# Kernel tuning notes

Measured on AMD Instinct MI355X. Metric: run time of the kernel, lower is better.

Reference implementation:

```python
import jax, jax.numpy as jnp
import numpy as np

NUM_CLASSES = 81
THRESHOLD = 0.5
NEGPOS_RATIO = 3
VARIANCE = (0.1, 0.2)


def point_form(p):
    # center-size -> corner form
    return jnp.concatenate([p[:, :2] - p[:, 2:] / 2, p[:, :2] + p[:, 2:] / 2], axis=1)


def jaccard(box_a, box_b):
    # box_a: [O,4] corners, box_b: [P,4] corners -> IoU [O,P]
    lt = jnp.maximum(box_a[:, None, :2], box_b[None, :, :2])
    rb = jnp.minimum(box_a[:, None, 2:], box_b[None, :, 2:])
    wh = jnp.clip(rb - lt, 0.0)
    inter = wh[..., 0] * wh[..., 1]
    area_a = ((box_a[:, 2] - box_a[:, 0]) * (box_a[:, 3] - box_a[:, 1]))[:, None]
    area_b = ((box_b[:, 2] - box_b[:, 0]) * (box_b[:, 3] - box_b[:, 1]))[None, :]
    return inter / (area_a + area_b - inter)


def encode(matched, priors, variances):
    # matched: [P,4] corner GT, priors: [P,4] center-size
    g_cxcy = (matched[:, :2] + matched[:, 2:]) / 2 - priors[:, :2]
    g_cxcy = g_cxcy / (variances[0] * priors[:, 2:])
    g_wh = (matched[:, 2:] - matched[:, :2]) / priors[:, 2:]
    g_wh = jnp.log(g_wh) / variances[1]
    return jnp.concatenate([g_cxcy, g_wh], axis=1)


def match_one(truths, labels, priors):
    overlaps = jaccard(truths, point_form(priors))   # [O,P]
    best_prior_idx = jnp.argmax(overlaps, axis=1)     # [O] best prior per truth
    best_truth_overlap = jnp.max(overlaps, axis=0)    # [P]
    best_truth_idx = jnp.argmax(overlaps, axis=0)     # [P] best truth per prior
    # force each truth's best prior to match that truth
    best_truth_overlap = best_truth_overlap.at[best_prior_idx].set(2.0)
    best_truth_idx = best_truth_idx.at[best_prior_idx].set(jnp.arange(truths.shape[0]))
    matched = truths[best_truth_idx]                  # [P,4]
    conf = labels[best_truth_idx].astype(jnp.int32) + 1
    conf = jnp.where(best_truth_overlap < THRESHOLD, 0, conf)
    loc = encode(matched, priors, VARIANCE)
    return loc, conf


def _loss(loc_data, conf_data, targets, priors):
    B, P, C = conf_data.shape
    loc_t, conf_t = jax.vmap(lambda t: match_one(t[:, :4], t[:, 4], priors))(targets)
    pos = conf_t > 0                                  # [B,P]
    # smooth-L1 (beta=1) over positive priors, sum reduction
    d = loc_data - loc_t
    sl1 = jnp.where(jnp.abs(d) < 1.0, 0.5 * d * d, jnp.abs(d) - 0.5)
    loss_l = jnp.sum(jnp.where(pos[..., None], sl1, 0.0))
    # per-prior CE used both for mining ranking and the final conf loss
    ce = jax.nn.logsumexp(conf_data, axis=-1) - jnp.take_along_axis(
        conf_data, conf_t[..., None], axis=-1)[..., 0]   # [B,P]
    # hard negative mining: zero positives, double argsort for rank
    loss_c_rank = jnp.where(pos, 0.0, ce)
    loss_idx = jnp.argsort(-loss_c_rank, axis=1)
    idx_rank = jnp.argsort(loss_idx, axis=1)
    num_pos = jnp.sum(pos, axis=1, keepdims=True)     # [B,1]
    num_neg = jnp.minimum(NEGPOS_RATIO * num_pos, P - 1)
    neg = idx_rank < num_neg
    sel = pos | neg
    loss_c = jnp.sum(jnp.where(sel, ce, 0.0))
    N = jnp.sum(num_pos).astype(loc_data.dtype)
    return loss_l / N, loss_c / N


def setup_inputs():
    key = jax.random.key(0)
    kl, kc, kb1, kb2, kll, kp1, kp2 = jax.random.split(key, 7)
    B, P, O, C = 64, 8732, 50, NUM_CLASSES
    loc_data = jax.random.normal(kl, (B, P, 4), jnp.float32)
    conf_data = jax.random.normal(kc, (B, P, C), jnp.float32)
    # valid GT boxes in corner form inside [0,1]
    cxcy = jax.random.uniform(kb1, (B, O, 2), minval=0.2, maxval=0.8)
    wh = jax.random.uniform(kb2, (B, O, 2), minval=0.05, maxval=0.3)
    boxes = jnp.concatenate([cxcy - wh / 2, cxcy + wh / 2], axis=-1)
    labels = jax.random.randint(kll, (B, O), 0, C - 1).astype(jnp.float32)
    targets = jnp.concatenate([boxes, labels[..., None]], axis=-1)  # [B,O,5]
    # priors in center-size form
    pcxcy = jax.random.uniform(kp1, (P, 2), minval=0.05, maxval=0.95)
    pwh = jax.random.uniform(kp2, (P, 2), minval=0.05, maxval=0.5)
    priors = jnp.concatenate([pcxcy, pwh], axis=-1)
    return {"loc_data": loc_data, "conf_data": conf_data, "targets": targets, "priors": priors}


def reference(loc_data, conf_data, targets, priors):
    return _loss(loc_data, conf_data, targets, priors)
```

## Files before the change

kernel.cpp:

```cpp
#include <hip/hip_runtime.h>
#include <float.h>

#pragma clang fp contract(off)

typedef unsigned long long ull;
typedef unsigned int u32;

#define THRESH 0.5f
#define PPT 4
#define CE_R 128
#define SEL_T 512
#define ENC_SEG 1024


__device__ __forceinline__ float sl1(float d) {
    float a = fabsf(d);
    return (a < 1.f) ? 0.5f * d * d : a - 0.5f;
}

__global__ __launch_bounds__(256) void k_prep(
        const float* __restrict__ targets, const float* __restrict__ priors,
        const float* __restrict__ conf,
        float* __restrict__ bto, int* __restrict__ bti, ull* __restrict__ tbest,
        float* __restrict__ lse,
        u32* __restrict__ zws, int nz,
        int P, int O, int S, int CB, int SB, int npairs, long long BP) {
    const int bid = blockIdx.x;
    __shared__ float4 tbox[128];
    __shared__ float tarea[128];
    __shared__ float s[CE_R * 81];
    if (bid < CB) {
        if (bid == 0)
            for (int i = threadIdx.x; i < nz; i += 256) zws[i] = 0;
        long long r0 = (long long)bid * CE_R;
        int nrow = (int)min((long long)CE_R, BP - r0);
        int nfl = nrow * 81;
        const float* src = conf + r0 * 81;
        int nv4 = nfl >> 2;
        for (int i = threadIdx.x; i < nv4; i += 256)
            ((float4*)s)[i] = ((const float4*)src)[i];
        for (int i = (nv4 << 2) + (int)threadIdx.x; i < nfl; i += 256)
            s[i] = src[i];
        __syncthreads();
        int row = threadIdx.x >> 1;
        int half = threadIdx.x & 1;
        if (row < nrow) {
            const float* rp = s + row * 81;
            int c0 = half * 41;
            int cn = half ? 40 : 41;
            float sum = 0.f;
            for (int j = 0; j < cn; j++) sum += __expf(rp[c0 + j]);
            sum += __shfl_xor(sum, 1);
            if (half == 0) lse[r0 + row] = __logf(sum);
        }
    } else if (bid < CB + SB) {
        const int ab = bid - CB;
        const int b = ab / S, seg = ab % S;
        const float* trow = targets + (size_t)b * O * 5;
        for (int o = threadIdx.x; o < O; o += 256) {
            float x1 = trow[o * 5 + 0], y1 = trow[o * 5 + 1];
            float x2 = trow[o * 5 + 2], y2 = trow[o * 5 + 3];
            tbox[o] = make_float4(x1, y1, x2, y2);
            tarea[o] = (x2 - x1) * (y2 - y1);
        }
        __syncthreads();
        const int p0 = seg * (256 * PPT);
        float px1[PPT], py1[PPT], px2[PPT], py2[PPT], pa[PPT];
        float bestv[PPT]; int besto[PPT]; int pidx[PPT];
#pragma unroll
        for (int j = 0; j < PPT; j++) {
            int p = p0 + (int)threadIdx.x + j * 256;
            pidx[j] = p; bestv[j] = -1.f; besto[j] = 0;
            if (p < P) {
                float4 pr = ((const float4*)priors)[p];
                px1[j] = pr.x - pr.z / 2.f;
                py1[j] = pr.y - pr.w / 2.f;
                px2[j] = pr.x + pr.z / 2.f;
                py2[j] = pr.y + pr.w / 2.f;
                pa[j] = (px2[j] - px1[j]) * (py2[j] - py1[j]);
            } else {
                px1[j] = 2.f; py1[j] = 2.f; px2[j] = 2.f; py2[j] = 2.f; pa[j] = 1.f;
            }
        }
        for (int o = 0; o < O; o++) {
            float4 t = tbox[o];
            float ta = tarea[o];
#pragma unroll
            for (int j = 0; j < PPT; j++) {
                float lx = fmaxf(t.x, px1[j]), ly = fmaxf(t.y, py1[j]);
                float rx = fminf(t.z, px2[j]), ry = fminf(t.w, py2[j]);
                float wx = fmaxf(rx - lx, 0.f), wy = fmaxf(ry - ly, 0.f);
                float inter = wx * wy;
                float iou = 0.f;
                if (inter > 0.f) iou = inter / (ta + pa[j] - inter);
                if (iou > bestv[j]) { bestv[j] = iou; besto[j] = o; }
            }
        }
#pragma unroll
        for (int j = 0; j < PPT; j++) {
            if (pidx[j] < P) {
                bto[(size_t)b * P + pidx[j]] = bestv[j];
                bti[(size_t)b * P + pidx[j]] = besto[j];
            }
        }
    } else {
        int g = (bid - CB - SB) * 4 + ((int)threadIdx.x >> 6);
        int lane = threadIdx.x & 63;
        if (g >= npairs) return;
        int OP = (O + 1) >> 1;
        int b = g / OP;
        int o0 = (g % OP) * 2;
        const float* trow = targets + ((size_t)b * O + o0) * 5;
        float ax1 = trow[0], ay1 = trow[1], ax2 = trow[2], ay2 = trow[3];
        float ta0 = (ax2 - ax1) * (ay2 - ay1);
        bool has1 = (o0 + 1) < O;
        float cx1 = 0, cy1 = 0, cx2 = 0, cy2 = 0, ta1 = 1.f;
        if (has1) {
            cx1 = trow[5]; cy1 = trow[6]; cx2 = trow[7]; cy2 = trow[8];
            ta1 = (cx2 - cx1) * (cy2 - cy1);
        }
        ull k0 = 0, k1 = 0;
        for (int p = lane; p < P; p += 64) {
            float4 pr = ((const float4*)priors)[p];
            float bx1 = pr.x - pr.z / 2.f;
            float by1 = pr.y - pr.w / 2.f;
            float bx2 = pr.x + pr.z / 2.f;
            float by2 = pr.y + pr.w / 2.f;
            float pa = (bx2 - bx1) * (by2 - by1);
            u32 np = ~(u32)p;
            {
                float lx = fmaxf(ax1, bx1), ly = fmaxf(ay1, by1);
                float rx = fminf(ax2, bx2), ry = fminf(ay2, by2);
                float wx = fmaxf(rx - lx, 0.f), wy = fmaxf(ry - ly, 0.f);
                float inter = wx * wy;
                float iou = 0.f;
                if (inter > 0.f) iou = inter / (ta0 + pa - inter);
                ull key = ((ull)__float_as_uint(iou) << 32) | np;
                if (key > k0) k0 = key;
            }
            if (has1) {
                float lx = fmaxf(cx1, bx1), ly = fmaxf(cy1, by1);
                float rx = fminf(cx2, bx2), ry = fminf(cy2, by2);
                float wx = fmaxf(rx - lx, 0.f), wy = fmaxf(ry - ly, 0.f);
                float inter = wx * wy;
                float iou = 0.f;
                if (inter > 0.f) iou = inter / (ta1 + pa - inter);
                ull key = ((ull)__float_as_uint(iou) << 32) | np;
                if (key > k1) k1 = key;
            }
        }
        for (int off = 32; off; off >>= 1) {
            ull a = __shfl_xor(k0, off); if (a > k0) k0 = a;
            ull d = __shfl_xor(k1, off); if (d > k1) k1 = d;
        }
        if (lane == 0) {
            tbest[(size_t)b * O + o0] = k0;
            if (has1) tbest[(size_t)b * O + o0 + 1] = k1;
        }
    }
}

__global__ __launch_bounds__(256) void k_encode_ce(
        const float* __restrict__ targets, const float* __restrict__ priors,
        const float* __restrict__ loc_data, const float* __restrict__ conf,
        const ull* __restrict__ tbest, const float* __restrict__ lse,
        float* __restrict__ F,
        int* __restrict__ conf_t,
        int* __restrict__ num_pos, float* __restrict__ loss_l,
        int P, int O) {
    const int b = blockIdx.y, seg = blockIdx.x;
    __shared__ float tr[64 * 5];
    __shared__ int ov[ENC_SEG];
    __shared__ float redf[4]; __shared__ int redi[4];
    const int p0 = seg * ENC_SEG;
    const int p1 = min(p0 + ENC_SEG, P);
    const int nprior = p1 - p0;
    const float* trow = targets + (size_t)b * O * 5;
    for (int i = threadIdx.x; i < O * 5; i += 256) tr[i] = trow[i];
    for (int i = threadIdx.x; i < nprior; i += 256) ov[i] = -1;
    __syncthreads();
    if ((int)threadIdx.x < O) {
        ull tb = tbest[(size_t)b * O + threadIdx.x];
        u32 p = ~(u32)(tb & 0xFFFFFFFFULL);
        if (p >= (u32)P) p = 0;
        if ((int)p >= p0 && (int)p < p1) atomicMax(&ov[p - p0], (int)threadIdx.x);
    }
    __syncthreads();
    float ll = 0.f; int cnt = 0;
    for (int p = p0 + (int)threadIdx.x; p < p1; p += 256) {
        size_t idx = (size_t)b * P + p;
        int o = conf_t[idx];
        int ovv = ov[p - p0];
        bool forced = ovv >= 0;
        if (forced) o = ovv;
        float ovl = F[idx];
        int cv = (!forced && ovl < THRESH) ? 0 : ((int)tr[o * 5 + 4] + 1);
        conf_t[idx] = cv;
        if (cv > 0) {
            cnt++;
            float4 pr = ((const float4*)priors)[p];
            float mx1 = tr[o * 5], my1 = tr[o * 5 + 1];
            float mx2 = tr[o * 5 + 2], my2 = tr[o * 5 + 3];
            float gx = ((mx1 + mx2) / 2.f - pr.x) / (0.1f * pr.z);
            float gy = ((my1 + my2) / 2.f - pr.y) / (0.1f * pr.w);
            float gw = logf((mx2 - mx1) / pr.z) / 0.2f;
            float gh = logf((my2 - my1) / pr.w) / 0.2f;
            float4 ld = ((const float4*)loc_data)[idx];
            ll += sl1(ld.x - gx) + sl1(ld.y - gy) + sl1(ld.z - gw) + sl1(ld.w - gh);
        }
        float tv = conf[idx * 81 + cv];
        F[idx] = lse[idx] - tv;
    }
    for (int off = 32; off; off >>= 1) {
        ll += __shfl_down(ll, off);
        cnt += __shfl_down(cnt, off);
    }
    int w = threadIdx.x >> 6;
    if ((threadIdx.x & 63) == 0) { redf[w] = ll; redi[w] = cnt; }
    __syncthreads();
    if (threadIdx.x == 0) {
        float l = 0; int c = 0;
        for (int i = 0; i < 4; i++) { l += redf[i]; c += redi[i]; }
        if (c) atomicAdd(&num_pos[b], c);
        atomicAdd(&loss_l[b], l);
    }
}

__global__ __launch_bounds__(SEL_T) void k_select(
        const float* __restrict__ ce, const int* __restrict__ conf_t,
        const int* __restrict__ num_pos, const float* __restrict__ loss_l,
        float* __restrict__ acc, u32* __restrict__ ticket,
        float* __restrict__ out, int P, int B) {
    extern __shared__ u32 sk[];
    __shared__ u32 whist[SEL_T / 64][16];
    __shared__ u32 hist[16];
    __shared__ float redf[SEL_T / 64]; __shared__ u32 redu[SEL_T / 64];
    __shared__ u32 sh_pval; __shared__ int sh_rem;
    const int b = blockIdx.x;
    const size_t base = (size_t)b * P;
    const int lane = threadIdx.x & 63;
    const int w = threadIdx.x >> 6;
    const int NW = SEL_T / 64;

    float ps = 0.f;
    for (int p = threadIdx.x; p < P; p += SEL_T) {
        int c = conf_t[base + p];
        float v = ce[base + p];
        u32 key;
        if (c > 0) { ps += v; key = 0u; }
        else key = __float_as_uint(fmaxf(v, 0.f));
        sk[p] = key;
    }
    for (int off = 32; off; off >>= 1) ps += __shfl_down(ps, off);
    if (lane == 0) redf[w] = ps;
    __syncthreads();
    float pos_sum = 0.f;
    if (threadIdx.x == 0) {
        for (int i = 0; i < NW; i++) pos_sum += redf[i];
    }

    const int np = num_pos[b];
    const int k = min(3 * np, P - 1);
    u32 pval = 0, pmask = 0; int rem = k;
    if (k > 0) {
        for (int shift = 28; shift >= 0; shift -= 4) {
            __syncthreads();
            ull a0 = 0, a1 = 0;
            for (int p = threadIdx.x; p < P; p += SEL_T) {
                u32 key = sk[p];
                if ((key & pmask) == pval) {
                    u32 dig = (key >> shift) & 15u;
                    ull inc = 1ull << ((dig & 7u) * 8u);
                    if (dig < 8u) a0 += inc; else a1 += inc;
                }
            }
            const ull M = 0x00FF00FF00FF00FFull;
            ull e0 = a0 & M, e1 = (a0 >> 8) & M, e2 = a1 & M, e3 = (a1 >> 8) & M;
            for (int off = 32; off; off >>= 1) {
                e0 += __shfl_xor(e0, off);
                e1 += __shfl_xor(e1, off);
                e2 += __shfl_xor(e2, off);
                e3 += __shfl_xor(e3, off);
            }
            if (lane == 0) {
#pragma unroll
                for (int j = 0; j < 4; j++) {
                    whist[w][2 * j]     = (u32)((e0 >> (16 * j)) & 0xFFFF);
                    whist[w][2 * j + 1] = (u32)((e1 >> (16 * j)) & 0xFFFF);
                    whist[w][8 + 2 * j]     = (u32)((e2 >> (16 * j)) & 0xFFFF);
                    whist[w][8 + 2 * j + 1] = (u32)((e3 >> (16 * j)) & 0xFFFF);
                }
            }
            __syncthreads();
            if (threadIdx.x < 16) {
                u32 h = 0;
                for (int i = 0; i < NW; i++) h += whist[i][threadIdx.x];
                hist[threadIdx.x] = h;
            }
            __syncthreads();
            if (threadIdx.x == 0) {
                u32 accu = 0; int d = 15;
                for (; d > 0; d--) {
                    u32 h = hist[d];
                    if (accu + h >= (u32)rem) break;
                    accu += h;
                }
                sh_pval = pval | ((u32)d << shift);
                sh_rem = rem - (int)accu;
            }
            __syncthreads();
            pval = sh_pval; rem = sh_rem; pmask |= (0xFu << shift);
        }
    }

    float sgt = 0.f; u32 cgt = 0;
    if (k > 0) {
        for (int p = threadIdx.x; p < P; p += SEL_T) {
            u32 key = sk[p];
            if (key > pval) { sgt += __uint_as_float(key); cgt++; }
        }
    }
    for (int off = 32; off; off >>= 1) {
        sgt += __shfl_down(sgt, off);
        cgt += __shfl_down(cgt, off);
    }
    __syncthreads();
    if (lane == 0) { redf[w] = sgt; redu[w] = cgt; }
    __syncthreads();
    if (threadIdx.x == 0) {
        float s = 0.f; u32 c = 0;
        for (int i = 0; i < NW; i++) { s += redf[i]; c += redu[i]; }
        float t = __uint_as_float(pval);
        float lc_b = pos_sum + ((k > 0) ? (s + (float)(k - (int)c) * t) : 0.f);
        atomicAdd(&acc[0], (float)np);
        atomicAdd(&acc[1], loss_l[b]);
        atomicAdd(&acc[2], lc_b);
        __threadfence();
        u32 tk = atomicAdd(ticket, 1u);
        if (tk == (u32)(B - 1)) {
            float n  = atomicAdd(&acc[0], 0.f);
            float ll = atomicAdd(&acc[1], 0.f);
            float lc = atomicAdd(&acc[2], 0.f);
            out[0] = ll / n;
            out[1] = lc / n;
        }
    }
}


extern "C" void kernel_launch(void* const* d_in, const int* in_sizes, int n_in,
                              void* d_out, int out_size, void* d_ws, size_t ws_size,
                              hipStream_t stream) {
    const float* loc     = (const float*)d_in[0];
    const float* conf    = (const float*)d_in[1];
    const float* targets = (const float*)d_in[2];
    const float* priors  = (const float*)d_in[3];

    const int P = in_sizes[3] / 4;
    const int B = in_sizes[0] / (P * 4);
    const int O = in_sizes[2] / (B * 5);
    const long long BP = (long long)B * P;

    char* ws = (char*)d_ws;
    size_t off = 0;
    int*   num_pos = (int*)(ws + off);   off += (size_t)B * sizeof(int);
    float* loss_l  = (float*)(ws + off); off += (size_t)B * sizeof(float);
    float* acc     = (float*)(ws + off); off += 4 * sizeof(float);
    u32*   ticket  = (u32*)(ws + off);   off += sizeof(u32);
    const int zwords = (int)(off >> 2);
    off = (off + 7) & ~(size_t)7;
    ull*   tbest   = (ull*)(ws + off);   off += (size_t)B * O * sizeof(ull);
    float* F       = (float*)(ws + off); off += (size_t)BP * sizeof(float);
    int*   I       = (int*)(ws + off);   off += (size_t)BP * sizeof(int);
    float* L       = (float*)(ws + off); off += (size_t)BP * sizeof(float);

    const int SEG = 256 * PPT;
    const int S = (P + SEG - 1) / SEG;
    const int SB = S * B;
    const int npairs = B * ((O + 1) / 2);
    const int TB = (npairs + 3) / 4;
    const int CB = (int)((BP + CE_R - 1) / CE_R);
    k_prep<<<CB + SB + TB, 256, 0, stream>>>(targets, priors, conf, F, I, tbest, L,
                                             (u32*)ws, zwords, P, O, S, CB, SB, npairs, BP);

    const int S2 = (P + ENC_SEG - 1) / ENC_SEG;
    k_encode_ce<<<dim3(S2, B), 256, 0, stream>>>(targets, priors, loc, conf, tbest, L,
                                                 F, I, num_pos, loss_l, P, O);

    k_select<<<B, SEL_T, (size_t)P * sizeof(u32), stream>>>(F, I, num_pos, loss_l,
                                                            acc, ticket, (float*)d_out, P, B);
}
```

Before: 390.6 us.

## Compute row LSE per thread from global memory and interleave IoU blocks

The log-sum-exp part of the prep kernel no longer stages 128 rows of confidence scores in about 41 KB of shared memory. Each thread now reads one 81-float row straight from global memory with float4 loads and sums the exponentials itself. The matching and per-truth argmax blocks are spread evenly across the grid instead of running after all the LSE blocks, so compute-heavy and memory-heavy work can overlap. Dropping the large shared buffer should raise occupancy. The cost is that lanes read rows 324 bytes apart, so loads are less coalesced, and the float4 loads are not 16-byte aligned.

```diff
diff --git a/kernel.cpp b/kernel.cpp
--- a/kernel.cpp
+++ b/kernel.cpp
@@ -8,7 +8,6 @@
 
 #define THRESH 0.5f
 #define PPT 4
-#define CE_R 128
 #define SEL_T 512
 #define ENC_SEG 1024
 
@@ -24,38 +23,44 @@
         float* __restrict__ bto, int* __restrict__ bti, ull* __restrict__ tbest,
         float* __restrict__ lse,
         u32* __restrict__ zws, int nz,
-        int P, int O, int S, int CB, int SB, int npairs, long long BP) {
+        int P, int O, int S, int SB, int SPEC, int G, int npairs, long long BP) {
     const int bid = blockIdx.x;
     __shared__ float4 tbox[128];
     __shared__ float tarea[128];
-    __shared__ float s[CE_R * 81];
-    if (bid < CB) {
-        if (bid == 0)
-            for (int i = threadIdx.x; i < nz; i += 256) zws[i] = 0;
-        long long r0 = (long long)bid * CE_R;
-        int nrow = (int)min((long long)CE_R, BP - r0);
-        int nfl = nrow * 81;
-        const float* src = conf + r0 * 81;
-        int nv4 = nfl >> 2;
-        for (int i = threadIdx.x; i < nv4; i += 256)
-            ((float4*)s)[i] = ((const float4*)src)[i];
-        for (int i = (nv4 << 2) + (int)threadIdx.x; i < nfl; i += 256)
-            s[i] = src[i];
-        __syncthreads();
-        int row = threadIdx.x >> 1;
-        int half = threadIdx.x & 1;
-        if (row < nrow) {
-            const float* rp = s + row * 81;
-            int c0 = half * 41;
-            int cn = half ? 40 : 41;
-            float sum = 0.f;
-            for (int j = 0; j < cn; j++) sum += __expf(rp[c0 + j]);
-            sum += __shfl_xor(sum, 1);
-            if (half == 0) lse[r0 + row] = __logf(sum);
-        }
-    } else if (bid < CB + SB) {
-        const int ab = bid - CB;
-        const int b = ab / S, seg = ab % S;
+    if (bid == 0)
+        for (int i = threadIdx.x; i < nz; i += 256) zws[i] = 0;
+
+    long long t0 = (long long)bid * SPEC;
+    int k0 = (int)(t0 / G);
+    bool is_spec = (int)((t0 + SPEC) / G) > k0;
+
+    if (!is_spec) {
+        int lb = bid - k0;
+        long long r = (long long)lb * 256 + threadIdx.x;
+        if (r < BP) {
+            const float* rp = conf + r * 81;
+            float s0 = 0.f, s1 = 0.f;
+#pragma unroll
+            for (int k = 0; k < 10; k++) {
+                float4 v = *(const float4*)(rp + 4 * k);
+                s0 += __expf(v.x); s0 += __expf(v.y);
+                s0 += __expf(v.z); s0 += __expf(v.w);
+            }
+            s0 += __expf(rp[40]);
+#pragma unroll
+            for (int k = 0; k < 10; k++) {
+                float4 v = *(const float4*)(rp + 41 + 4 * k);
+                s1 += __expf(v.x); s1 += __expf(v.y);
+                s1 += __expf(v.z); s1 += __expf(v.w);
+            }
+            lse[r] = __logf(s0 + s1);
+        }
+        return;
+    }
+
+    const int sidx = k0;
+    if (sidx < SB) {
+        const int b = sidx / S, seg = sidx % S;
         const float* trow = targets + (size_t)b * O * 5;
         for (int o = threadIdx.x; o < O; o += 256) {
             float x1 = trow[o * 5 + 0], y1 = trow[o * 5 + 1];
@@ -104,7 +109,7 @@
             }
         }
     } else {
-        int g = (bid - CB - SB) * 4 + ((int)threadIdx.x >> 6);
+        int g = (sidx - SB) * 4 + ((int)threadIdx.x >> 6);
         int lane = threadIdx.x & 63;
         if (g >= npairs) return;
         int OP = (O + 1) >> 1;
@@ -119,7 +124,7 @@
             cx1 = trow[5]; cy1 = trow[6]; cx2 = trow[7]; cy2 = trow[8];
             ta1 = (cx2 - cx1) * (cy2 - cy1);
         }
-        ull k0 = 0, k1 = 0;
+        ull k0v = 0, k1v = 0;
         for (int p = lane; p < P; p += 64) {
             float4 pr = ((const float4*)priors)[p];
             float bx1 = pr.x - pr.z / 2.f;
@@ -136,7 +141,7 @@
                 float iou = 0.f;
                 if (inter > 0.f) iou = inter / (ta0 + pa - inter);
                 ull key = ((ull)__float_as_uint(iou) << 32) | np;
-                if (key > k0) k0 = key;
+                if (key > k0v) k0v = key;
             }
             if (has1) {
                 float lx = fmaxf(cx1, bx1), ly = fmaxf(cy1, by1);
@@ -146,16 +151,16 @@
                 float iou = 0.f;
                 if (inter > 0.f) iou = inter / (ta1 + pa - inter);
                 ull key = ((ull)__float_as_uint(iou) << 32) | np;
-                if (key > k1) k1 = key;
+                if (key > k1v) k1v = key;
             }
         }
         for (int off = 32; off; off >>= 1) {
-            ull a = __shfl_xor(k0, off); if (a > k0) k0 = a;
-            ull d = __shfl_xor(k1, off); if (d > k1) k1 = d;
+            ull a = __shfl_xor(k0v, off); if (a > k0v) k0v = a;
+            ull d = __shfl_xor(k1v, off); if (d > k1v) k1v = d;
         }
         if (lane == 0) {
-            tbest[(size_t)b * O + o0] = k0;
-            if (has1) tbest[(size_t)b * O + o0 + 1] = k1;
+            tbest[(size_t)b * O + o0] = k0v;
+            if (has1) tbest[(size_t)b * O + o0 + 1] = k1v;
         }
     }
 }
@@ -379,9 +384,11 @@
     const int SB = S * B;
     const int npairs = B * ((O + 1) / 2);
     const int TB = (npairs + 3) / 4;
-    const int CB = (int)((BP + CE_R - 1) / CE_R);
-    k_prep<<<CB + SB + TB, 256, 0, stream>>>(targets, priors, conf, F, I, tbest, L,
-                                             (u32*)ws, zwords, P, O, S, CB, SB, npairs, BP);
+    const int CB = (int)((BP + 255) / 256);
+    const int SPEC = SB + TB;
+    const int G = CB + SPEC;
+    k_prep<<<G, 256, 0, stream>>>(targets, priors, conf, F, I, tbest, L,
+                                  (u32*)ws, zwords, P, O, S, SB, SPEC, G, npairs, BP);
 
     const int S2 = (P + ENC_SEG - 1) / ENC_SEG;
     k_encode_ce<<<dim3(S2, B), 256, 0, stream>>>(targets, priors, loc, conf, tbest, L,
```

Result: faster. 368.4 us (-5.7%).
